# Kernel tuning notes

Hardware: AMD Instinct MI355X
Metric: run time of the kernel (lower is better)

## Reference

```python
import jax, jax.numpy as jnp
import numpy as np

B, S, D, H, DK, DV, SEG = 2, 4096, 1024, 8, 128, 128, 512
NSEG = S // SEG


def setup_inputs() -> dict:
    key = jax.random.key(0)
    k0, k1, k2, k3, k4, k5 = jax.random.split(key, 6)
    return {
        "x": jax.random.normal(k0, (B, S, D), jnp.float32),
        "Wk": jax.random.normal(k1, (H, D, DK), jnp.float32) / np.float32(np.sqrt(D)),
        "Wv": jax.random.normal(k2, (H, D, DV), jnp.float32) / np.float32(np.sqrt(D)),
        "Wq": jax.random.normal(k3, (H, D, DK), jnp.float32) / np.float32(np.sqrt(D)),
        "Wout": jax.random.normal(k4, (H * DV, D), jnp.float32) / np.float32(np.sqrt(H * DV)),
        "betas": jax.random.normal(k5, (1, H, 1, DV), jnp.float32),
    }


def reference(x, Wk, Wv, Wq, Wout, betas):
    # Per-head projections: (B,H,S,dk/dv)
    k_full = jnp.einsum('bsd,hdk->bhsk', x, Wk)
    v_full = jnp.einsum('bsd,hdk->bhsk', x, Wv)
    q_full = jnp.einsum('bsd,hdk->bhsk', x, Wq)

    def to_segs(t):  # (B,H,S,E) -> (NSEG,B,H,SEG,E)
        return t.reshape(B, H, NSEG, SEG, t.shape[-1]).transpose(2, 0, 1, 3, 4)

    segs = (to_segs(k_full), to_segs(v_full), to_segs(q_full))

    mem0 = jnp.zeros((B, H, DK, DV), x.dtype)           # compressive memory
    z0 = jnp.full((B, H, DK, 1), 1.0 / DK, x.dtype)     # normalizer
    causal_mask = jnp.tril(jnp.ones((SEG, SEG), bool))
    gate = jax.nn.sigmoid(betas)                        # (1,H,1,DV)
    scale = jnp.asarray(1.0 / np.sqrt(DK), x.dtype)

    def step(carry, seg):
        mem, z = carry
        k, v, q = seg                                   # (B,H,SEG,dk/dv)
        sigma_q = jax.nn.elu(q) + 1.0
        # segment-local causal softmax attention
        scores = jnp.einsum('bhik,bhjk->bhij', q, k) * scale
        scores = jnp.where(causal_mask, scores, -jnp.inf)
        att_dot = jax.nn.softmax(scores, axis=-1) @ v
        # linear-attention read from memory
        att_mem = (sigma_q @ mem) / (sigma_q @ z)
        # delta-rule memory update
        sigma_k = jax.nn.elu(k) + 1.0
        mem = mem + jnp.einsum('bhsk,bhsv->bhkv', sigma_k, v - (sigma_k @ mem) / (sigma_k @ z))
        z = z + jnp.sum(sigma_k, axis=-2, keepdims=True).swapaxes(-1, -2)
        # gated mix of memory and local attention
        att = gate * att_mem + (1.0 - gate) * att_dot   # (B,H,SEG,DV)
        att = att.transpose(0, 2, 1, 3).reshape(B, SEG, H * DV)
        return (mem, z), att @ Wout                     # (B,SEG,D)

    _, outs = jax.lax.scan(step, (mem0, z0), segs)      # (NSEG,B,SEG,D)
    return outs.transpose(1, 0, 2, 3).reshape(B, S, D)
```

## Files before the change

### kernel.cpp

```cpp
#include <hip/hip_runtime.h>

#define B_  2
#define S_  4096
#define D_  1024
#define H_  8
#define DK_ 128
#define DV_ 128
#define SEG_ 512
#define NSEG_ 8
#define BH_ 16
#define M_ 8192

typedef __attribute__((ext_vector_type(8))) short bf16x8;
typedef __attribute__((ext_vector_type(4))) float f32x4;

__device__ __forceinline__ float elu1(float x) { return x > 0.f ? x + 1.f : __expf(x); }
__device__ __forceinline__ float sigmoidf(float x) { return 1.f / (1.f + __expf(-x)); }

__device__ __forceinline__ unsigned short f2b(float f) {
    union { float f; unsigned int u; } x; x.f = f;
    unsigned int r = x.u + 0x7fffu + ((x.u >> 16) & 1u);
    return (unsigned short)(r >> 16);
}
__device__ __forceinline__ float b2f(unsigned short u) {
    union { unsigned int u; float f; } x; x.u = ((unsigned int)u) << 16; return x.f;
}

__device__ __forceinline__ void gl2lds16(const void* g, void* l) {
    __builtin_amdgcn_global_load_lds(
        (const __attribute__((address_space(1))) void*)g,
        (__attribute__((address_space(3))) void*)l, 16, 0, 0);
}

__global__ __launch_bounds__(256) void conv_bf16(
    const float* __restrict__ src, unsigned short* __restrict__ dst)
{
    int i = (blockIdx.x * 256 + threadIdx.x) * 4;
    float4 v = *(const float4*)(src + i);
    ushort4 o;
    o.x = f2b(v.x); o.y = f2b(v.y); o.z = f2b(v.z); o.w = f2b(v.w);
    *(ushort4*)(dst + i) = o;
}

__global__ __launch_bounds__(256) void transpose_conv(
    const float* __restrict__ src, unsigned short* __restrict__ dst, int R, int C)
{
    __shared__ float tile[32][33];
    const size_t moff = (size_t)blockIdx.z * R * C;
    src += moff; dst += moff;
    const int c0 = blockIdx.x * 32, r0 = blockIdx.y * 32;
    const int tx = threadIdx.x & 31, ty = threadIdx.x >> 5;
    #pragma unroll
    for (int i = 0; i < 32; i += 8)
        tile[ty + i][tx] = src[(size_t)(r0 + ty + i) * C + c0 + tx];
    __syncthreads();
    #pragma unroll
    for (int i = 0; i < 32; i += 8)
        dst[(size_t)(c0 + ty + i) * R + r0 + tx] = f2b(tile[tx][ty + i]);
}

__global__ __launch_bounds__(256) void transpose_conv3(
    const float* __restrict__ Wk, const float* __restrict__ Wv,
    const float* __restrict__ Wq, unsigned short* __restrict__ dst)
{
    __shared__ float tile[32][33];
    const int z = blockIdx.z;
    const int w = z >> 3;
    const float* src = (w == 0) ? Wk : (w == 1) ? Wv : Wq;
    src += (size_t)(z & 7) * 131072;
    dst += (size_t)z * 131072;
    const int c0 = blockIdx.x * 32, r0 = blockIdx.y * 32;
    const int tx = threadIdx.x & 31, ty = threadIdx.x >> 5;
    #pragma unroll
    for (int i = 0; i < 32; i += 8)
        tile[ty + i][tx] = src[(size_t)(r0 + ty + i) * 128 + c0 + tx];
    __syncthreads();
    #pragma unroll
    for (int i = 0; i < 32; i += 8)
        dst[(size_t)(c0 + ty + i) * 1024 + r0 + tx] = f2b(tile[tx][ty + i]);
}

__global__ __launch_bounds__(256) void colsum_k(
    const unsigned short* __restrict__ Kbb, float* __restrict__ colsum)
{
    __shared__ float red[32][128];
    const int t = threadIdx.x;
    const int bh = blockIdx.x >> 3, seg = blockIdx.x & 7;
    const unsigned short* Kp = Kbb + ((size_t)bh * 4096 + seg * 512) * 128;
    const int rbase = t >> 3, c0 = (t & 7) * 16;
    float part[16] = {};
    for (int chunk = 0; chunk < 16; ++chunk) {
        const unsigned short* p = Kp + (size_t)(chunk * 32 + rbase) * 128 + c0;
        bf16x8 a = *(const bf16x8*)p;
        bf16x8 b = *(const bf16x8*)(p + 8);
        #pragma unroll
        for (int j = 0; j < 8; ++j) {
            part[j]     += elu1(b2f((unsigned short)a[j]));
            part[j + 8] += elu1(b2f((unsigned short)b[j]));
        }
    }
    #pragma unroll
    for (int j = 0; j < 16; ++j) red[rbase][c0 + j] = part[j];
    __syncthreads();
    if (t < 128) {
        float s = 0.f;
        #pragma unroll
        for (int r = 0; r < 32; ++r) s += red[r][t];
        colsum[(size_t)blockIdx.x * 128 + t] = s;
    }
}

__global__ __launch_bounds__(256) void den_z(
    const unsigned short* __restrict__ Kbb, const float* __restrict__ colsum,
    float* __restrict__ den, float* __restrict__ zseg)
{
    __shared__ float zs[128];
    const int t = threadIdx.x;
    const int bh = blockIdx.x >> 3, seg = blockIdx.x & 7;
    if (t < 128) {
        float z = 1.f / 128.f;
        for (int j = 0; j < seg; ++j) z += colsum[(size_t)(bh * 8 + j) * 128 + t];
        zs[t] = z;
        zseg[(size_t)blockIdx.x * 128 + t] = z;
    }
    __syncthreads();
    #pragma unroll
    for (int rr = 0; rr < 2; ++rr) {
        int s = t + rr * 256;
        const unsigned short* kp = Kbb + ((size_t)bh * 4096 + seg * 512 + s) * 128;
        float d = 0.f;
        #pragma unroll 4
        for (int f = 0; f < 16; ++f) {
            bf16x8 a = *(const bf16x8*)(kp + f * 8);
            #pragma unroll
            for (int j = 0; j < 8; ++j)
                d += elu1(b2f((unsigned short)a[j])) * zs[f * 8 + j];
        }
        den[(size_t)bh * 4096 + seg * 512 + s] = d;
    }
}

__global__ __launch_bounds__(256) void sigma_kT2(
    const unsigned short* __restrict__ Kbb, const float* __restrict__ den,
    unsigned short* __restrict__ SkT, unsigned short* __restrict__ SkTs)
{
    __shared__ float tile[32][33];
    __shared__ float rden[32];
    const int bh = blockIdx.z;
    const int s0 = blockIdx.x * 32, dk0 = blockIdx.y * 32;
    const int tx = threadIdx.x & 31, ty = threadIdx.x >> 5;
    if (threadIdx.x < 32) rden[threadIdx.x] = 1.f / den[(size_t)bh * 4096 + s0 + threadIdx.x];
    #pragma unroll
    for (int i = 0; i < 32; i += 8)
        tile[ty + i][tx] = elu1(b2f(Kbb[((size_t)bh * 4096 + s0 + ty + i) * 128 + dk0 + tx]));
    __syncthreads();
    #pragma unroll
    for (int i = 0; i < 32; i += 8) {
        float v = tile[tx][ty + i];
        size_t o = ((size_t)bh * 128 + dk0 + ty + i) * 4096 + s0 + tx;
        SkT[o]  = f2b(v);
        SkTs[o] = f2b(v * rden[tx]);
    }
}

__device__ __forceinline__ void mfma_gemm_128_d1(
    const unsigned short* __restrict__ A, int lda,
    const unsigned short* __restrict__ Bt, int ldb, int K,
    unsigned short* As, unsigned short* Bs, f32x4 acc[4][4])
{
    const int tid = threadIdx.x;
    const int wave = tid >> 6, lane = tid & 63;
    const int r4 = lane >> 2;
    const int c4s = (((lane & 3) ^ ((lane >> 2) & 3)) * 8);
    const int lrow = lane & 15, lquad = lane >> 4;
    const int sl8 = (lquad ^ (lrow & 3)) * 8;
    const int wm = (wave >> 1) * 64, wn = (wave & 1) * 64;
    const int ar0 = wave * 32, ar1 = wave * 32 + 16;
    const int T = K >> 5;

    auto STAGE = [&](int t, int bufidx) {
        unsigned short* Ab = As + bufidx * 4096;
        unsigned short* Bb = Bs + bufidx * 4096;
        const int kk = t * 32;
        gl2lds16(A  + (size_t)(ar0 + r4) * lda + kk + c4s, Ab + ar0 * 32);
        gl2lds16(A  + (size_t)(ar1 + r4) * lda + kk + c4s, Ab + ar1 * 32);
        gl2lds16(Bt + (size_t)(ar0 + r4) * ldb + kk + c4s, Bb + ar0 * 32);
        gl2lds16(Bt + (size_t)(ar1 + r4) * ldb + kk + c4s, Bb + ar1 * 32);
    };

    STAGE(0, 0);
    for (int t = 0; t < T; ++t) {
        if (t + 1 < T) {
            STAGE(t + 1, (t + 1) & 1);
            asm volatile("s_waitcnt vmcnt(4)" ::: "memory");
        } else {
            asm volatile("s_waitcnt vmcnt(0)" ::: "memory");
        }
        __builtin_amdgcn_s_barrier();
        __builtin_amdgcn_sched_barrier(0);
        const unsigned short* Ac = As + (t & 1) * 4096;
        const unsigned short* Bc = Bs + (t & 1) * 4096;
        bf16x8 af[4], bfr[4];
        #pragma unroll
        for (int i = 0; i < 4; ++i)
            af[i] = *(const bf16x8*)(Ac + (wm + i * 16 + lrow) * 32 + sl8);
        #pragma unroll
        for (int j = 0; j < 4; ++j)
            bfr[j] = *(const bf16x8*)(Bc + (wn + j * 16 + lrow) * 32 + sl8);
        #pragma unroll
        for (int i = 0; i < 4; ++i)
            #pragma unroll
            for (int j = 0; j < 4; ++j)
                acc[i][j] = __builtin_amdgcn_mfma_f32_16x16x32_bf16(af[i], bfr[j], acc[i][j], 0, 0, 0);
        __builtin_amdgcn_s_barrier();
        __builtin_amdgcn_sched_barrier(0);
    }
}

__device__ __forceinline__ void mfma_gemm_128(
    const unsigned short* __restrict__ A, int lda,
    const unsigned short* __restrict__ Bt, int ldb, int K,
    unsigned short* As, unsigned short* Bs, f32x4 acc[4][4])
{
    const int tid = threadIdx.x;
    const int wave = tid >> 6, lane = tid & 63;
    const int r4 = lane >> 2;
    const int c4s = (((lane & 3) ^ ((lane >> 2) & 3)) * 8);
    const int lrow = lane & 15, lquad = lane >> 4;
    const int sl8 = (lquad ^ (lrow & 3)) * 8;
    const int wm = (wave >> 1) * 64, wn = (wave & 1) * 64;
    const int ar0 = wave * 32, ar1 = wave * 32 + 16;
    const int T = K >> 5;

    auto STAGE = [&](int t, int bufidx) {
        unsigned short* Ab = As + bufidx * 4096;
        unsigned short* Bb = Bs + bufidx * 4096;
        const int kk = t * 32;
        gl2lds16(A  + (size_t)(ar0 + r4) * lda + kk + c4s, Ab + ar0 * 32);
        gl2lds16(A  + (size_t)(ar1 + r4) * lda + kk + c4s, Ab + ar1 * 32);
        gl2lds16(Bt + (size_t)(ar0 + r4) * ldb + kk + c4s, Bb + ar0 * 32);
        gl2lds16(Bt + (size_t)(ar1 + r4) * ldb + kk + c4s, Bb + ar1 * 32);
    };

    STAGE(0, 0);
    STAGE(1, 1);
    int cur = 0;
    for (int t = 0; t < T; ++t) {
        if (t + 2 < T) {
            int nb = cur + 2; if (nb >= 3) nb -= 3;
            STAGE(t + 2, nb);
            asm volatile("s_waitcnt vmcnt(8)" ::: "memory");
        } else if (t + 1 < T) {
            asm volatile("s_waitcnt vmcnt(4)" ::: "memory");
        } else {
            asm volatile("s_waitcnt vmcnt(0)" ::: "memory");
        }
        __builtin_amdgcn_s_barrier();
        __builtin_amdgcn_sched_barrier(0);
        const unsigned short* Ac = As + cur * 4096;
        const unsigned short* Bc = Bs + cur * 4096;
        bf16x8 af[4], bfr[4];
        #pragma unroll
        for (int i = 0; i < 4; ++i)
            af[i] = *(const bf16x8*)(Ac + (wm + i * 16 + lrow) * 32 + sl8);
        #pragma unroll
        for (int j = 0; j < 4; ++j)
            bfr[j] = *(const bf16x8*)(Bc + (wn + j * 16 + lrow) * 32 + sl8);
        #pragma unroll
        for (int i = 0; i < 4; ++i)
            #pragma unroll
            for (int j = 0; j < 4; ++j)
                acc[i][j] = __builtin_amdgcn_mfma_f32_16x16x32_bf16(af[i], bfr[j], acc[i][j], 0, 0, 0);
        __builtin_amdgcn_s_barrier();
        __builtin_amdgcn_sched_barrier(0);
        cur += 1; if (cur >= 3) cur -= 3;
    }
}

__global__ __launch_bounds__(256) void gemm_qkv_mfma(
    const unsigned short* __restrict__ xb, const unsigned short* __restrict__ Wtb,
    unsigned short* __restrict__ Qbb, unsigned short* __restrict__ Kbb,
    unsigned short* __restrict__ Vtb)
{
    __shared__ unsigned short As[2 * 128 * 32];
    __shared__ unsigned short Bs[2 * 128 * 32];
    const int m0 = blockIdx.x * 128;
    const int panel = blockIdx.y;
    const int which = panel >> 3, h = panel & 7;
    f32x4 acc[4][4] = {};
    mfma_gemm_128_d1(xb + (size_t)m0 * 1024, 1024,
                     Wtb + (size_t)panel * 128 * 1024, 1024, 1024, As, Bs, acc);
    const int tid = threadIdx.x, wave = tid >> 6, lane = tid & 63;
    const int lrow = lane & 15, lquad = lane >> 4;
    const int wm = (wave >> 1) * 64, wn = (wave & 1) * 64;
    if (which == 1) {
        #pragma unroll
        for (int i = 0; i < 4; ++i) {
            int mb = m0 + wm + i * 16 + lquad * 4;
            int bb = mb >> 12, sb = mb & 4095;
            int bh = bb * 8 + h;
            size_t vbase = ((size_t)bh * 8 + (sb >> 9)) * 128;
            #pragma unroll
            for (int j = 0; j < 4; ++j) {
                int col = wn + j * 16 + lrow;
                ushort4 o;
                o.x = f2b(acc[i][j][0]); o.y = f2b(acc[i][j][1]);
                o.z = f2b(acc[i][j][2]); o.w = f2b(acc[i][j][3]);
                *(ushort4*)(Vtb + ((vbase + col) * 512 + (sb & 511))) = o;
            }
        }
    } else {
        unsigned short* Dst = (which == 0) ? Kbb : Qbb;
        #pragma unroll
        for (int i = 0; i < 4; ++i)
            #pragma unroll
            for (int r = 0; r < 4; ++r) {
                int m = m0 + wm + i * 16 + lquad * 4 + r;
                int bb = m >> 12, s = m & 4095;
                int bh = bb * 8 + h;
                size_t rowbase = ((size_t)bh * 4096 + s) * 128;
                #pragma unroll
                for (int j = 0; j < 4; ++j)
                    Dst[rowbase + wn + j * 16 + lrow] = f2b(acc[i][j][r]);
            }
    }
}

__global__ __launch_bounds__(256) void gemm_out_mfma(
    const unsigned short* __restrict__ A, const unsigned short* __restrict__ Bt,
    float* __restrict__ C)
{
    __shared__ unsigned short As[2 * 128 * 32];
    __shared__ unsigned short Bs[2 * 128 * 32];
    const int m0 = blockIdx.x * 128, n0 = blockIdx.y * 128;
    f32x4 acc[4][4] = {};
    mfma_gemm_128_d1(A + (size_t)m0 * 1024, 1024,
                     Bt + (size_t)n0 * 1024, 1024, 1024, As, Bs, acc);
    const int tid = threadIdx.x, wave = tid >> 6, lane = tid & 63;
    const int lrow = lane & 15, lquad = lane >> 4;
    const int wm = (wave >> 1) * 64, wn = (wave & 1) * 64;
    #pragma unroll
    for (int i = 0; i < 4; ++i)
        #pragma unroll
        for (int r = 0; r < 4; ++r) {
            int m = m0 + wm + i * 16 + lquad * 4 + r;
            #pragma unroll
            for (int j = 0; j < 4; ++j)
                C[(size_t)m * 1024 + n0 + wn + j * 16 + lrow] = acc[i][j][r];
        }
}

__global__ __launch_bounds__(256) void ac_gemm(
    const unsigned short* __restrict__ SkT, const unsigned short* __restrict__ SkTs,
    const unsigned short* __restrict__ Vtb,
    unsigned short* __restrict__ Emat, float* __restrict__ Cmat)
{
    __shared__ unsigned short As[3 * 128 * 32];
    __shared__ unsigned short Bs[3 * 128 * 32];
    const int pair = blockIdx.x >> 1, which = blockIdx.x & 1;
    const int bh = pair >> 3, seg = pair & 7;
    const unsigned short* Ap = SkT + (size_t)bh * 128 * 4096 + seg * 512;
    const unsigned short* Bp = which
        ? (Vtb  + (size_t)pair * 128 * 512)
        : (SkTs + (size_t)bh * 128 * 4096 + seg * 512);
    const int ldb = which ? 512 : 4096;
    f32x4 acc[4][4] = {};
    mfma_gemm_128(Ap, 4096, Bp, ldb, 512, As, Bs, acc);
    const int tid = threadIdx.x, wave = tid >> 6, lane = tid & 63;
    const int lrow = lane & 15, lquad = lane >> 4;
    const int wm = (wave >> 1) * 64, wn = (wave & 1) * 64;
    if (which == 0) {
        #pragma unroll
        for (int i = 0; i < 4; ++i)
            #pragma unroll
            for (int r = 0; r < 4; ++r) {
                int m = wm + i * 16 + lquad * 4 + r;
                #pragma unroll
                for (int j = 0; j < 4; ++j)
                    Emat[(size_t)pair * 16384 + (size_t)m * 128 + wn + j * 16 + lrow]
                        = f2b(-acc[i][j][r]);
            }
    } else {
        #pragma unroll
        for (int i = 0; i < 4; ++i)
            #pragma unroll
            for (int r = 0; r < 4; ++r) {
                int m = wm + i * 16 + lquad * 4 + r;
                #pragma unroll
                for (int j = 0; j < 4; ++j)
                    Cmat[(size_t)pair * 16384 + (size_t)m * 128 + wn + j * 16 + lrow]
                        = acc[i][j][r];
            }
    }
}

__global__ __launch_bounds__(512) void scan_step(
    const unsigned short* __restrict__ Emat, const float* __restrict__ Cmat,
    unsigned short* __restrict__ Memb)
{
    __shared__ unsigned short msh[128][136];
    const int t = threadIdx.x;
    const int wv = t >> 6, lane = t & 63;
    const int n16 = lane & 15, quad = lane >> 4;
    const int bh = blockIdx.x;
    f32x4 macc[8] = {};
    for (int seg = 0; seg < 8; ++seg) {
        unsigned short* gm = Memb + ((size_t)(bh * 8 + seg)) * 16384;
        #pragma unroll
        for (int vt = 0; vt < 8; ++vt) {
            ushort4 o;
            o.x = f2b(macc[vt][0]); o.y = f2b(macc[vt][1]);
            o.z = f2b(macc[vt][2]); o.w = f2b(macc[vt][3]);
            *(ushort4*)&msh[vt * 16 + n16][wv * 16 + quad * 4] = o;
            *(ushort4*)(gm + (size_t)(vt * 16 + n16) * 128 + wv * 16 + quad * 4) = o;
        }
        if (seg == 7) break;
        __syncthreads();
        const unsigned short* Ep = Emat + ((size_t)(bh * 8 + seg)) * 16384
                                 + (size_t)(wv * 16 + n16) * 128;
        bf16x8 ea[4];
        #pragma unroll
        for (int kf = 0; kf < 4; ++kf)
            ea[kf] = *(const bf16x8*)(Ep + kf * 32 + quad * 8);
        const float* Cp = Cmat + ((size_t)(bh * 8 + seg)) * 16384
                        + (size_t)(wv * 16 + quad * 4) * 128;
        #pragma unroll
        for (int vt = 0; vt < 8; ++vt)
            #pragma unroll
            for (int r = 0; r < 4; ++r)
                macc[vt][r] += Cp[(size_t)r * 128 + vt * 16 + n16];
        #pragma unroll
        for (int vt = 0; vt < 8; ++vt)
            #pragma unroll
            for (int kf = 0; kf < 4; ++kf) {
                bf16x8 bfr = *(const bf16x8*)&msh[vt * 16 + n16][kf * 32 + quad * 8];
                macc[vt] = __builtin_amdgcn_mfma_f32_16x16x32_bf16(ea[kf], bfr, macc[vt], 0, 0, 0);
            }
        __syncthreads();
    }
}

__global__ __launch_bounds__(256) void attn_out(
    const unsigned short* __restrict__ Qbb, const unsigned short* __restrict__ Kbb,
    const unsigned short* __restrict__ Vtb, const unsigned short* __restrict__ Memb,
    const float* __restrict__ zseg, const float* __restrict__ betas,
    unsigned short* __restrict__ Attb)
{
    __shared__ unsigned short Pl[4][32][72];
    const int tid = threadIdx.x, wave = tid >> 6, lane = tid & 63;
    const int n = lane & 15, quad = lane >> 4;
    const int bh = blockIdx.x >> 3, seg = blockIdx.x & 7;
    const int a = blockIdx.y;
    const int qt = (wave < 2) ? a : 7 - a;
    const int sp = (wave & 1) * 2;
    const int b = bh >> 3, h = bh & 7;
    const float scale2 = 0.12751744979f;
    const float FSH2 = 23.083120654f;

    const unsigned short* Qp = Qbb + ((size_t)bh * 4096 + seg * 512 + qt * 64 + sp * 16) * 128;
    const unsigned short* Kp = Kbb + ((size_t)bh * 4096 + seg * 512) * 128;
    const unsigned short* Vp = Vtb + ((size_t)bh * 8 + seg) * 128 * 512;

    bf16x8 aQ[2][4];
    #pragma unroll
    for (int s = 0; s < 2; ++s)
        #pragma unroll
        for (int kc = 0; kc < 4; ++kc)
            aQ[s][kc] = *(const bf16x8*)(Qp + (size_t)(s * 16 + n) * 128 + kc * 32 + quad * 8);

    f32x4 O[2][8] = {};
    float lpart[2][4] = {};

    for (int jt = 0; jt <= qt; ++jt) {
        f32x4 Sf[2][4] = {};
        #pragma unroll
        for (int kc = 0; kc < 4; ++kc) {
            bf16x8 bK[4];
            #pragma unroll
            for (int ns = 0; ns < 4; ++ns)
                bK[ns] = *(const bf16x8*)(Kp + (size_t)(jt * 64 + ns * 16 + n) * 128 + kc * 32 + quad * 8);
            #pragma unroll
            for (int ns = 0; ns < 4; ++ns) {
                Sf[0][ns] = __builtin_amdgcn_mfma_f32_16x16x32_bf16(aQ[0][kc], bK[ns], Sf[0][ns], 0, 0, 0);
                Sf[1][ns] = __builtin_amdgcn_mfma_f32_16x16x32_bf16(aQ[1][kc], bK[ns], Sf[1][ns], 0, 0, 0);
            }
        }
        const bool diag = (jt == qt);
        #pragma unroll
        for (int s = 0; s < 2; ++s)
            #pragma unroll
            for (int reg = 0; reg < 4; ++reg) {
                #pragma unroll
                for (int ns = 0; ns < 4; ++ns) {
                    float sv = Sf[s][ns][reg] * scale2 - FSH2;
                    if (diag) {
                        int grow = qt * 64 + (sp + s) * 16 + quad * 4 + reg;
                        int gcol = jt * 64 + ns * 16 + n;
                        if (gcol > grow) sv = -1e30f;
                    }
                    float p = exp2f(sv);
                    lpart[s][reg] += p;
                    Pl[wave][s * 16 + quad * 4 + reg][ns * 16 + n] = f2b(p);
                }
            }
        bf16x8 aP[2][2];
        #pragma unroll
        for (int s = 0; s < 2; ++s) {
            aP[s][0] = *(const bf16x8*)&Pl[wave][s * 16 + n][quad * 8];
            aP[s][1] = *(const bf16x8*)&Pl[wave][s * 16 + n][32 + quad * 8];
        }
        #pragma unroll
        for (int dvs = 0; dvs < 8; ++dvs) {
            bf16x8 bV0 = *(const bf16x8*)(Vp + (size_t)(dvs * 16 + n) * 512 + jt * 64 + quad * 8);
            bf16x8 bV1 = *(const bf16x8*)(Vp + (size_t)(dvs * 16 + n) * 512 + jt * 64 + 32 + quad * 8);
            O[0][dvs] = __builtin_amdgcn_mfma_f32_16x16x32_bf16(aP[0][0], bV0, O[0][dvs], 0, 0, 0);
            O[0][dvs] = __builtin_amdgcn_mfma_f32_16x16x32_bf16(aP[0][1], bV1, O[0][dvs], 0, 0, 0);
            O[1][dvs] = __builtin_amdgcn_mfma_f32_16x16x32_bf16(aP[1][0], bV0, O[1][dvs], 0, 0, 0);
            O[1][dvs] = __builtin_amdgcn_mfma_f32_16x16x32_bf16(aP[1][1], bV1, O[1][dvs], 0, 0, 0);
        }
    }
    const float* zp = zseg + (size_t)(bh * 8 + seg) * 128;
    const unsigned short* Mp = Memb + (size_t)(bh * 8 + seg) * 16384;
    #pragma unroll
    for (int s = 0; s < 2; ++s) {
        float l_i[4];
        #pragma unroll
        for (int r = 0; r < 4; ++r) {
            float rs = lpart[s][r];
            rs += __shfl_xor(rs, 1);
            rs += __shfl_xor(rs, 2);
            rs += __shfl_xor(rs, 4);
            rs += __shfl_xor(rs, 8);
            l_i[r] = rs;
        }
        float den = 0.f;
        bf16x8 aS[4];
        #pragma unroll
        for (int kc = 0; kc < 4; ++kc) {
            float4 z0 = *(const float4*)(zp + kc * 32 + quad * 8);
            float4 z1 = *(const float4*)(zp + kc * 32 + quad * 8 + 4);
            float zv[8] = {z0.x, z0.y, z0.z, z0.w, z1.x, z1.y, z1.z, z1.w};
            bf16x8 aa;
            #pragma unroll
            for (int j = 0; j < 8; ++j) {
                float sv = elu1(b2f((unsigned short)aQ[s][kc][j]));
                den += sv * zv[j];
                aa[j] = (short)f2b(sv);
            }
            aS[kc] = aa;
        }
        den += __shfl_xor(den, 16);
        den += __shfl_xor(den, 32);
        f32x4 Om[8] = {};
        #pragma unroll
        for (int dvs = 0; dvs < 8; ++dvs)
            #pragma unroll
            for (int kc = 0; kc < 4; ++kc) {
                bf16x8 bm = *(const bf16x8*)(Mp + (size_t)(dvs * 16 + n) * 128 + kc * 32 + quad * 8);
                Om[dvs] = __builtin_amdgcn_mfma_f32_16x16x32_bf16(aS[kc], bm, Om[dvs], 0, 0, 0);
            }
        float irm[4], inv[4];
        #pragma unroll
        for (int r = 0; r < 4; ++r) {
            irm[r] = 1.f / __shfl(den, quad * 4 + r);
            inv[r] = 1.f / l_i[r];
        }
        #pragma unroll
        for (int dvs = 0; dvs < 8; ++dvs) {
            int dv = dvs * 16 + n;
            float g = sigmoidf(betas[h * 128 + dv]);
            #pragma unroll
            for (int r = 0; r < 4; ++r) {
                int srow = seg * 512 + qt * 64 + (sp + s) * 16 + quad * 4 + r;
                float val = g * Om[dvs][r] * irm[r] + (1.f - g) * O[s][dvs][r] * inv[r];
                Attb[((size_t)b * 4096 + srow) * 1024 + h * 128 + dv] = f2b(val);
            }
        }
    }
}

extern "C" void kernel_launch(void* const* d_in, const int* in_sizes, int n_in,
                              void* d_out, int out_size, void* d_ws, size_t ws_size,
                              hipStream_t stream) {
    const float* x     = (const float*)d_in[0];
    const float* Wk    = (const float*)d_in[1];
    const float* Wv    = (const float*)d_in[2];
    const float* Wq    = (const float*)d_in[3];
    const float* Wout  = (const float*)d_in[4];
    const float* betas = (const float*)d_in[5];
    float* out = (float*)d_out;

    unsigned short* Qbb  = (unsigned short*)d_ws;
    unsigned short* Kbb  = Qbb + 8388608;
    unsigned short* Vtb  = Kbb + 8388608;
    unsigned short* SkT  = Vtb + 8388608;
    unsigned short* SkTs = SkT + 8388608;
    unsigned short* Emat = SkTs + 8388608;
    unsigned short* Memb = Emat + 2097152;
    float* Cmat   = (float*)(Memb + 2097152);
    float* colsum = Cmat + 2097152;
    float* zseg   = colsum + 16384;
    float* den    = zseg + 16384;
    unsigned short* xb    = SkT;
    unsigned short* Wtb   = SkTs;
    unsigned short* Attb  = SkT;
    unsigned short* Woutb = SkTs;

    conv_bf16<<<8192, 256, 0, stream>>>(x, xb);
    transpose_conv3<<<dim3(4, 32, 24), 256, 0, stream>>>(Wk, Wv, Wq, Wtb);
    gemm_qkv_mfma<<<dim3(64, 24), 256, 0, stream>>>(xb, Wtb, Qbb, Kbb, Vtb);
    colsum_k<<<128, 256, 0, stream>>>(Kbb, colsum);
    den_z<<<128, 256, 0, stream>>>(Kbb, colsum, den, zseg);
    sigma_kT2<<<dim3(128, 4, 16), 256, 0, stream>>>(Kbb, den, SkT, SkTs);
    ac_gemm<<<256, 256, 0, stream>>>(SkT, SkTs, Vtb, Emat, Cmat);
    scan_step<<<16, 512, 0, stream>>>(Emat, Cmat, Memb);
    attn_out<<<dim3(128, 4), 256, 0, stream>>>(Qbb, Kbb, Vtb, Memb, zseg, betas, Attb);
    transpose_conv<<<dim3(32, 32, 1), 256, 0, stream>>>(Wout, Woutb, 1024, 1024);
    gemm_out_mfma<<<dim3(64, 8), 256, 0, stream>>>(Attb, Woutb, out);
}
```

Measured before the change: 362.0 us.

## Load QKV GEMM B operand directly into registers and triple-buffer A tiles

The QKV projection GEMM gets a new mainloop. The weight operand is loaded straight from global memory into registers, double-buffered in registers, and the A operand goes through LDS with a three-stage ring buffer and deeper prefetch. The output projection GEMM moves from the double-buffered mainloop to the existing triple-buffered one. The goal is to cut LDS traffic and barrier stalls and hide global latency better, in exchange for more registers and more LDS per block in the output GEMM, which can lower occupancy.

```diff
diff --git a/kernel.cpp b/kernel.cpp
--- a/kernel.cpp
+++ b/kernel.cpp
@@ -160,60 +160,6 @@
         size_t o = ((size_t)bh * 128 + dk0 + ty + i) * 4096 + s0 + tx;
         SkT[o]  = f2b(v);
         SkTs[o] = f2b(v * rden[tx]);
-    }
-}
-
-__device__ __forceinline__ void mfma_gemm_128_d1(
-    const unsigned short* __restrict__ A, int lda,
-    const unsigned short* __restrict__ Bt, int ldb, int K,
-    unsigned short* As, unsigned short* Bs, f32x4 acc[4][4])
-{
-    const int tid = threadIdx.x;
-    const int wave = tid >> 6, lane = tid & 63;
-    const int r4 = lane >> 2;
-    const int c4s = (((lane & 3) ^ ((lane >> 2) & 3)) * 8);
-    const int lrow = lane & 15, lquad = lane >> 4;
-    const int sl8 = (lquad ^ (lrow & 3)) * 8;
-    const int wm = (wave >> 1) * 64, wn = (wave & 1) * 64;
-    const int ar0 = wave * 32, ar1 = wave * 32 + 16;
-    const int T = K >> 5;
-
-    auto STAGE = [&](int t, int bufidx) {
-        unsigned short* Ab = As + bufidx * 4096;
-        unsigned short* Bb = Bs + bufidx * 4096;
-        const int kk = t * 32;
-        gl2lds16(A  + (size_t)(ar0 + r4) * lda + kk + c4s, Ab + ar0 * 32);
-        gl2lds16(A  + (size_t)(ar1 + r4) * lda + kk + c4s, Ab + ar1 * 32);
-        gl2lds16(Bt + (size_t)(ar0 + r4) * ldb + kk + c4s, Bb + ar0 * 32);
-        gl2lds16(Bt + (size_t)(ar1 + r4) * ldb + kk + c4s, Bb + ar1 * 32);
-    };
-
-    STAGE(0, 0);
-    for (int t = 0; t < T; ++t) {
-        if (t + 1 < T) {
-            STAGE(t + 1, (t + 1) & 1);
-            asm volatile("s_waitcnt vmcnt(4)" ::: "memory");
-        } else {
-            asm volatile("s_waitcnt vmcnt(0)" ::: "memory");
-        }
-        __builtin_amdgcn_s_barrier();
-        __builtin_amdgcn_sched_barrier(0);
-        const unsigned short* Ac = As + (t & 1) * 4096;
-        const unsigned short* Bc = Bs + (t & 1) * 4096;
-        bf16x8 af[4], bfr[4];
-        #pragma unroll
-        for (int i = 0; i < 4; ++i)
-            af[i] = *(const bf16x8*)(Ac + (wm + i * 16 + lrow) * 32 + sl8);
-        #pragma unroll
-        for (int j = 0; j < 4; ++j)
-            bfr[j] = *(const bf16x8*)(Bc + (wn + j * 16 + lrow) * 32 + sl8);
-        #pragma unroll
-        for (int i = 0; i < 4; ++i)
-            #pragma unroll
-            for (int j = 0; j < 4; ++j)
-                acc[i][j] = __builtin_amdgcn_mfma_f32_16x16x32_bf16(af[i], bfr[j], acc[i][j], 0, 0, 0);
-        __builtin_amdgcn_s_barrier();
-        __builtin_amdgcn_sched_barrier(0);
     }
 }
 
@@ -277,19 +223,86 @@
     }
 }
 
+__device__ __forceinline__ void mfma_gemm_128_bd(
+    const unsigned short* __restrict__ A, int lda,
+    const unsigned short* __restrict__ Bt, int ldb, int K,
+    unsigned short* As, f32x4 acc[4][4])
+{
+    const int tid = threadIdx.x;
+    const int wave = tid >> 6, lane = tid & 63;
+    const int r4 = lane >> 2;
+    const int c4s = (((lane & 3) ^ ((lane >> 2) & 3)) * 8);
+    const int lrow = lane & 15, lquad = lane >> 4;
+    const int sl8 = (lquad ^ (lrow & 3)) * 8;
+    const int wm = (wave >> 1) * 64, wn = (wave & 1) * 64;
+    const int ar0 = wave * 32, ar1 = wave * 32 + 16;
+    const int T = K >> 5;
+
+    auto STAGE_A = [&](int t, int bufidx) {
+        unsigned short* Ab = As + bufidx * 4096;
+        const int kk = t * 32;
+        gl2lds16(A + (size_t)(ar0 + r4) * lda + kk + c4s, Ab + ar0 * 32);
+        gl2lds16(A + (size_t)(ar1 + r4) * lda + kk + c4s, Ab + ar1 * 32);
+    };
+    auto LOADB = [&](int t, bf16x8 (&dst)[4]) {
+        const int kk = t * 32;
+        #pragma unroll
+        for (int j = 0; j < 4; ++j)
+            dst[j] = *(const bf16x8*)(Bt + (size_t)(wn + j * 16 + lrow) * ldb + kk + lquad * 8);
+    };
+
+    bf16x8 bB[4], bBn[4];
+    STAGE_A(0, 0);
+    STAGE_A(1, 1);
+    LOADB(0, bB);
+    int cur = 0;
+
+    auto KSTEP = [&](int t, bf16x8 (&bu)[4], bf16x8 (&bp)[4]) {
+        if (t + 1 < T) LOADB(t + 1, bp);
+        if (t + 2 < T) {
+            int nb = cur + 2; if (nb >= 3) nb -= 3;
+            STAGE_A(t + 2, nb);
+            asm volatile("s_waitcnt vmcnt(12)" ::: "memory");
+        } else if (t + 1 < T) {
+            asm volatile("s_waitcnt vmcnt(10)" ::: "memory");
+        } else {
+            asm volatile("s_waitcnt vmcnt(0)" ::: "memory");
+        }
+        __builtin_amdgcn_s_barrier();
+        __builtin_amdgcn_sched_barrier(0);
+        const unsigned short* Ac = As + cur * 4096;
+        bf16x8 af[4];
+        #pragma unroll
+        for (int i = 0; i < 4; ++i)
+            af[i] = *(const bf16x8*)(Ac + (wm + i * 16 + lrow) * 32 + sl8);
+        #pragma unroll
+        for (int i = 0; i < 4; ++i)
+            #pragma unroll
+            for (int j = 0; j < 4; ++j)
+                acc[i][j] = __builtin_amdgcn_mfma_f32_16x16x32_bf16(af[i], bu[j], acc[i][j], 0, 0, 0);
+        __builtin_amdgcn_s_barrier();
+        __builtin_amdgcn_sched_barrier(0);
+        cur += 1; if (cur >= 3) cur -= 3;
+    };
+
+    for (int t = 0; t < T; t += 2) {
+        KSTEP(t,     bB,  bBn);
+        KSTEP(t + 1, bBn, bB);
+    }
+}
+
 __global__ __launch_bounds__(256) void gemm_qkv_mfma(
     const unsigned short* __restrict__ xb, const unsigned short* __restrict__ Wtb,
     unsigned short* __restrict__ Qbb, unsigned short* __restrict__ Kbb,
     unsigned short* __restrict__ Vtb)
 {
-    __shared__ unsigned short As[2 * 128 * 32];
-    __shared__ unsigned short Bs[2 * 128 * 32];
+    __shared__ unsigned short As[3 * 128 * 32];
     const int m0 = blockIdx.x * 128;
     const int panel = blockIdx.y;
     const int which = panel >> 3, h = panel & 7;
     f32x4 acc[4][4] = {};
-    mfma_gemm_128_d1(xb + (size_t)m0 * 1024, 1024,
-                     Wtb + (size_t)panel * 128 * 1024, 1024, 1024, As, Bs, acc);
+    mfma_gemm_128_bd(xb + (size_t)m0 * 1024, 1024,
+                     Wtb + (size_t)panel * 128 * 1024, 1024, 1024, As, acc);
     const int tid = threadIdx.x, wave = tid >> 6, lane = tid & 63;
     const int lrow = lane & 15, lquad = lane >> 4;
     const int wm = (wave >> 1) * 64, wn = (wave & 1) * 64;
@@ -330,12 +343,12 @@
     const unsigned short* __restrict__ A, const unsigned short* __restrict__ Bt,
     float* __restrict__ C)
 {
-    __shared__ unsigned short As[2 * 128 * 32];
-    __shared__ unsigned short Bs[2 * 128 * 32];
+    __shared__ unsigned short As[3 * 128 * 32];
+    __shared__ unsigned short Bs[3 * 128 * 32];
     const int m0 = blockIdx.x * 128, n0 = blockIdx.y * 128;
     f32x4 acc[4][4] = {};
-    mfma_gemm_128_d1(A + (size_t)m0 * 1024, 1024,
-                     Bt + (size_t)n0 * 1024, 1024, 1024, As, Bs, acc);
+    mfma_gemm_128(A + (size_t)m0 * 1024, 1024,
+                  Bt + (size_t)n0 * 1024, 1024, 1024, As, Bs, acc);
     const int tid = threadIdx.x, wave = tid >> 6, lane = tid & 63;
     const int lrow = lane & 15, lquad = lane >> 4;
     const int wm = (wave >> 1) * 64, wn = (wave & 1) * 64;
```

New measurement: 392.2 us. +8.3%, slower.
